# Performance work log

Hardware: AMD Instinct MI355X
Metric: run time of the kernel (lower is better)

## Reference

```python
import jax, jax.numpy as jnp
import numpy as np

L, N, HID, HEADS, BLK = 4096, 2, 1024, 16, 64
RAND_NUM = 2


def setup_inputs() -> dict:
    key = jax.random.key(0)
    ks = jax.random.split(key, 11)
    s = 0.02
    nb = L // BLK
    return {
        "query": jax.random.normal(ks[0], (L, N, HID), jnp.float32),
        "q_proj": jax.random.normal(ks[1], (HID, HID), jnp.float32) * s,
        "q_bias": jax.random.normal(ks[2], (HID,), jnp.float32) * s,
        "k_proj": jax.random.normal(ks[3], (HID, HID), jnp.float32) * s,
        "k_bias": jax.random.normal(ks[4], (HID,), jnp.float32) * s,
        "v_proj": jax.random.normal(ks[5], (HID, HID), jnp.float32) * s,
        "v_bias": jax.random.normal(ks[6], (HID,), jnp.float32) * s,
        "out_proj": jax.random.normal(ks[7], (HID, HID), jnp.float32) * s,
        "out_bias": jax.random.normal(ks[8], (HID,), jnp.float32) * s,
        "rand_indices": jax.random.randint(ks[9], (nb - 2, RAND_NUM), 2, nb, jnp.int64 if jax.config.jax_enable_x64 else jnp.int32),
        "h": HEADS,
        "block_size": BLK,
    }


def reference(query, q_proj, q_bias, k_proj, k_bias, v_proj, v_bias,
              out_proj, out_bias, rand_indices, h, block_size):
    Lq, Nb, hidden = query.shape
    dh = hidden // h
    b = block_size
    nb = Lq // b
    Z = Nb * h  # batch*heads leading dim
    scale = dh ** -0.5

    lin = lambda x, w, bi: x @ w.T + bi
    # [L, N, hidden] -> [N*h, L, dh]
    q = lin(query, q_proj, q_bias).reshape(Lq, Z, dh).transpose(1, 0, 2) * scale
    k = lin(query, k_proj, k_bias).reshape(Lq, Z, dh).transpose(1, 0, 2)
    v = lin(query, v_proj, v_bias).reshape(Lq, Z, dh).transpose(1, 0, 2)

    qb = q.reshape(Z, nb, b, dh)
    kb = k.reshape(Z, nb, b, dh)
    vb = v.reshape(Z, nb, b, dh)

    # ---- global blocks: first 2 blocks of queries attend to everything;
    #      all middle queries attend to first 2 key blocks ----
    head = jnp.einsum('zqd,zkd->zqk', q[:, :2 * b], k)          # [Z, 2b, L]
    col = jnp.einsum('zqd,zkd->zqk', q[:, 2 * b:], k[:, :2 * b])  # [Z, L-2b, 2b]

    # ---- sliding window (3 neighboring blocks), bottom row zero-padded ----
    skeys = jnp.concatenate([kb[:, 1:-2], kb[:, 2:-1], kb[:, 3:]], axis=2)  # [Z, nb-3, 3b, dh]
    sbot_k = jnp.concatenate([jnp.zeros_like(kb[:, -1:]), kb[:, -2:-1], kb[:, -1:]], axis=2)
    skeys = jnp.concatenate([skeys, sbot_k], axis=1)            # [Z, nb-2, 3b, dh]
    sqk = jnp.einsum('znqd,znkd->znqk', qb[:, 2:], skeys)
    sqk = sqk.reshape(Z, (nb - 2) * b, 3 * b)

    # ---- random blocks (rand_num per query block) ----
    gk = kb[:, rand_indices].reshape(Z, nb - 2, RAND_NUM * b, dh)
    rqk = jnp.einsum('znqd,znkd->znqk', qb[:, 2:], gk)
    rqk = rqk.reshape(Z, (nb - 2) * b, RAND_NUM * b)

    middle = jnp.concatenate([col, sqk, rqk], axis=-1)          # [Z, L-2b, 7b]

    head_attn = jax.nn.softmax(head, axis=-1)
    mid_attn = jax.nn.softmax(middle, axis=-1)

    # ---- attn @ v ----
    head_out = jnp.einsum('zqk,zkd->zqd', head_attn, v)          # [Z, 2b, dh]
    mid_out = jnp.einsum('zqk,zkd->zqd', mid_attn[:, :, :2 * b], v[:, :2 * b])

    svals = jnp.concatenate([vb[:, 1:-2], vb[:, 2:-1], vb[:, 3:]], axis=2)
    sbot_v = jnp.concatenate([vb[:, -2:-1], vb[:, -1:], jnp.zeros_like(vb[:, -1:])], axis=2)
    svals = jnp.concatenate([svals, sbot_v], axis=1)             # [Z, nb-2, 3b, dh]
    ms = mid_attn[:, :, 2 * b:5 * b].reshape(Z, nb - 2, b, 3 * b)
    mid_out = mid_out + jnp.einsum('znqk,znkd->znqd', ms, svals).reshape(Z, (nb - 2) * b, dh)

    gv = vb[:, rand_indices].reshape(Z, nb - 2, RAND_NUM * b, dh)
    mr = mid_attn[:, :, 5 * b:].reshape(Z, nb - 2, b, RAND_NUM * b)
    mid_out = mid_out + jnp.einsum('znqk,znkd->znqd', mr, gv).reshape(Z, (nb - 2) * b, dh)

    out = jnp.concatenate([head_out, mid_out], axis=1)           # [Z, L, dh]
    out = out.transpose(1, 0, 2).reshape(Lq, Nb, hidden)
    return lin(out, out_proj, out_bias)
```

## Files before the change

kernel.cpp:

```cpp
#include <hip/hip_runtime.h>
#include <stdint.h>

#define L_SEQ 4096
#define NBATCH 2
#define HID 1024
#define HEADS 16
#define DH 64
#define Z_DIM 32
#define NBLK 64
#define NROWS 8192
#define NSPLIT 8

typedef float f32x4 __attribute__((ext_vector_type(4)));
typedef short short8 __attribute__((ext_vector_type(8)));

typedef const uint32_t __attribute__((address_space(1))) *gas_ptr;
typedef uint32_t __attribute__((address_space(3))) *las_ptr;

__device__ __forceinline__ ushort f2bf(float f) {
  uint32_t u = __float_as_uint(f);
  uint32_t r = (u + 0x7FFFu + ((u >> 16) & 1u)) >> 16;
  return (ushort)r;
}

__device__ __forceinline__ void gload_lds16(const void* g, void* l) {
  __builtin_amdgcn_global_load_lds((gas_ptr)g, (las_ptr)l, 16, 0, 0);
}

__global__ __launch_bounds__(256)
void cvt_multi(const float* __restrict__ s0, ushort* __restrict__ d0,
               const float* __restrict__ s1, ushort* __restrict__ d1,
               const float* __restrict__ s2, ushort* __restrict__ d2,
               const float* __restrict__ s3, ushort* __restrict__ d3,
               const float* __restrict__ s4, ushort* __restrict__ d4) {
  const int i = blockIdx.x * blockDim.x + threadIdx.x;
  const int NQ = NROWS * HID / 4;
  const float4* src; ushort4* dst; int off;
  if (i < NQ) {
    src = (const float4*)s0; dst = (ushort4*)d0; off = i;
  } else {
    const int j = i - NQ;
    const int r = j >> 18;
    off = j & ((1 << 18) - 1);
    src = (const float4*)(r == 0 ? s1 : r == 1 ? s2 : r == 2 ? s3 : s4);
    dst = (ushort4*)(r == 0 ? d1 : r == 1 ? d2 : r == 2 ? d3 : d4);
  }
  float4 v = src[off];
  ushort4 o;
  o.x = f2bf(v.x); o.y = f2bf(v.y); o.z = f2bf(v.z); o.w = f2bf(v.w);
  dst[off] = o;
}

template <int FINAL>
__global__ __launch_bounds__(256)
void gemm_bt(const ushort* __restrict__ X,
             const ushort* __restrict__ W0, const ushort* __restrict__ W1,
             const ushort* __restrict__ W2,
             const float* __restrict__ b0, const float* __restrict__ b1,
             const float* __restrict__ b2,
             ushort* __restrict__ Qo, ushort* __restrict__ Ko,
             ushort* __restrict__ Vo, float* __restrict__ Fo) {
  const int tid = threadIdx.x;
  const int w = tid >> 6, l = tid & 63;
  const int lr = l & 15, lg = l >> 4;
  const int wr = w >> 1, wc = w & 1;

  const int total = FINAL ? 512 : 1536;
  const int per = total >> 3;
  const int f0 = blockIdx.x;
  const int nf = (f0 & 7) * per + (f0 >> 3);
  const int bx = nf & 7;
  const int by = (nf >> 3) & 63;
  const int zid = FINAL ? 0 : (nf >> 9);
  const int mbase = by * 128;
  const int nbase = bx * 128;

  const ushort* W = FINAL ? W0 : (zid == 0 ? W0 : (zid == 1 ? W1 : W2));
  const float*  B = FINAL ? b0 : (zid == 0 ? b0 : (zid == 1 ? b1 : b2));

  __shared__ ushort lds[2][8192];

  const int kch = (lg ^ ((lr >> 1) & 3)) << 3;

  f32x4 acc[4][4];
#pragma unroll
  for (int m = 0; m < 4; ++m)
#pragma unroll
    for (int n = 0; n < 4; ++n) acc[m][n] = (f32x4){0.f, 0.f, 0.f, 0.f};

  auto stage = [&](int k0, int buf) {
#pragma unroll
    for (int s = 0; s < 2; ++s) {
      const int chunk = s * 256 + tid;
      const int row = chunk >> 2, cc = chunk & 3;
      const int scc = cc ^ ((row >> 1) & 3);
      gload_lds16(X + (size_t)(mbase + row) * HID + k0 + scc * 8,
                  &lds[buf][(s * 256 + (tid & ~63)) * 8]);
      gload_lds16(W + (size_t)(nbase + row) * HID + k0 + scc * 8,
                  &lds[buf][4096 + (s * 256 + (tid & ~63)) * 8]);
    }
  };

  auto compute_tile = [&](const ushort* lA, const ushort* lB) {
    short8 af[4], bfr[4];
#pragma unroll
    for (int m = 0; m < 4; ++m)
      af[m] = *(const short8*)&lA[(wr * 64 + m * 16 + lr) * 32 + kch];
#pragma unroll
    for (int n = 0; n < 4; ++n)
      bfr[n] = *(const short8*)&lB[(wc * 64 + n * 16 + lr) * 32 + kch];
#pragma unroll
    for (int m = 0; m < 4; ++m)
#pragma unroll
      for (int n = 0; n < 4; ++n)
        acc[m][n] = __builtin_amdgcn_mfma_f32_16x16x32_bf16(af[m], bfr[n], acc[m][n], 0, 0, 0);
  };

  stage(0, 0);
  stage(32, 1);
  for (int t = 0; t < 32; ++t) {
    if (t < 30) { asm volatile("s_waitcnt vmcnt(4)" ::: "memory"); }
    else        { asm volatile("s_waitcnt vmcnt(0)" ::: "memory"); }
    __builtin_amdgcn_s_barrier();
    __builtin_amdgcn_sched_barrier(0);
    compute_tile(&lds[t & 1][0], &lds[t & 1][4096]);
    __builtin_amdgcn_sched_barrier(0);
    asm volatile("s_waitcnt lgkmcnt(0)" ::: "memory");
    __builtin_amdgcn_s_barrier();
    if (t < 30) stage((t + 2) * 32, t & 1);
  }

  if (FINAL) {
#pragma unroll
    for (int n = 0; n < 4; ++n) {
      const int col = nbase + wc * 64 + n * 16 + lr;
      const float bias = B[col];
#pragma unroll
      for (int m = 0; m < 4; ++m)
#pragma unroll
        for (int r = 0; r < 4; ++r) {
          const int row = mbase + wr * 64 + m * 16 + 4 * lg + r;
          Fo[(size_t)row * HID + col] = acc[m][n][r] + bias;
        }
    }
    return;
  }

  float biasn[4];
#pragma unroll
  for (int n = 0; n < 4; ++n) biasn[n] = B[nbase + wc * 64 + n * 16 + lr];
  ushort* st = &lds[0][0];

  if (zid == 2) {
#pragma unroll
    for (int nb2 = 0; nb2 < 2; ++nb2) {
#pragma unroll
      for (int ch = 0; ch < 2; ++ch) {
        __syncthreads();
        if (wc == ch) {
#pragma unroll
          for (int m = 0; m < 4; ++m)
#pragma unroll
            for (int n = 0; n < 4; ++n)
#pragma unroll
              for (int rr = 0; rr < 2; ++rr) {
                const int r = nb2 + 2 * rr;
                st[(n * 16 + lr) * 72 + wr * 32 + m * 8 + 2 * lg + rr] =
                    f2bf(acc[m][n][r] + biasn[n]);
              }
        }
        __syncthreads();
        const int zz = nb2 * HEADS + (nbase >> 6) + ch;
#pragma unroll
        for (int it = 0; it < 2; ++it) {
          const int c = it * 256 + tid;
          const int colI = c >> 3, ls0 = (c & 7) * 8;
          const short8 v = *(const short8*)&st[colI * 72 + ls0];
          *(short8*)&Vo[((size_t)zz * DH + colI) * L_SEQ + (mbase >> 1) + ls0] = v;
        }
      }
    }
  } else {
    ushort* Out = (zid == 0) ? Qo : Ko;
    const float sc = (zid == 0) ? 0.125f : 1.f;
#pragma unroll
    for (int nbp = 0; nbp < 2; ++nbp) {
#pragma unroll
      for (int hh = 0; hh < 2; ++hh) {
        __syncthreads();
        if (wc == hh) {
#pragma unroll
          for (int m = 0; m < 4; ++m)
#pragma unroll
            for (int n = 0; n < 4; ++n)
#pragma unroll
              for (int rr = 0; rr < 2; ++rr) {
                const int r = nbp + 2 * rr;
                st[(wr * 32 + m * 8 + 2 * lg + rr) * 72 + n * 16 + lr] =
                    f2bf((acc[m][n][r] + biasn[n]) * sc);
              }
        }
        __syncthreads();
        const int zz = nbp * HEADS + (nbase >> 6) + hh;
#pragma unroll
        for (int it = 0; it < 2; ++it) {
          const int c = it * 256 + tid;
          const int lr2 = c >> 3, cc8 = c & 7;
          const short8 v = *(const short8*)&st[lr2 * 72 + cc8 * 8];
          *(short8*)&Out[((size_t)zz * L_SEQ + (mbase >> 1) + lr2) * DH + cc8 * 8] = v;
        }
      }
    }
  }
}

__global__ __launch_bounds__(256)
void attn_sparse(const ushort* __restrict__ Q, const ushort* __restrict__ K,
                 const ushort* __restrict__ Vt, const int* __restrict__ rnd,
                 ushort* __restrict__ O,
                 float* __restrict__ Pp, float* __restrict__ Mp,
                 float* __restrict__ Lp) {
  const int bid = blockIdx.x;
  int z, qb, split = 0;
  bool head;
  if (bid < Z_DIM * 62) {
    z = bid / 62; qb = bid % 62 + 2; head = false;
  } else {
    const int t = bid - Z_DIM * 62;
    z = t >> 4; qb = (t >> 3) & 1; split = t & 7; head = true;
  }
  const int tid = threadIdx.x;
  const int w = tid >> 6, l = tid & 63;
  const int lr = l & 15, lg = l >> 4;

  __shared__ ushort Kl[64 * 64];
  __shared__ ushort Vl[64 * 64];
  __shared__ ushort Pl[4][16 * 64];

  const ushort* Qbase = Q + ((size_t)z * L_SEQ + qb * 64 + w * 16) * DH;
  const short8 aq0 = *(const short8*)(Qbase + lr * DH + lg * 8);
  const short8 aq1 = *(const short8*)(Qbase + lr * DH + 32 + lg * 8);

  float m[4], lsum[4];
  f32x4 accO[4];
#pragma unroll
  for (int r = 0; r < 4; ++r) { m[r] = -1e30f; lsum[r] = 0.f; }
#pragma unroll
  for (int t = 0; t < 4; ++t) accO[t] = (f32x4){0.f, 0.f, 0.f, 0.f};

  const int nslot = head ? 8 : 7;
  int sk[3] = {0, 0, 0}, sv[3] = {0, 0, 0}, rk0 = 0, rk1 = 0;
  if (!head) {
    const int i = qb - 2;
    rk0 = rnd[2 * i]; rk1 = rnd[2 * i + 1];
    if (qb < NBLK - 1) {
      sk[0] = qb - 1; sk[1] = qb; sk[2] = qb + 1;
      sv[0] = qb - 1; sv[1] = qb; sv[2] = qb + 1;
    } else {
      sk[0] = -1; sk[1] = NBLK - 2; sk[2] = NBLK - 1;
      sv[0] = NBLK - 2; sv[1] = NBLK - 1; sv[2] = -1;
    }
  }

  for (int slot = 0; slot < nslot; ++slot) {
    int ki, vi;
    if (head) { ki = split * 8 + slot; vi = ki; }
    else if (slot < 2) { ki = slot; vi = slot; }
    else if (slot < 5) { ki = sk[slot - 2]; vi = sv[slot - 2]; }
    else { ki = (slot == 5) ? rk0 : rk1; vi = ki; }

    if (slot) __syncthreads();
#pragma unroll
    for (int s = 0; s < 2; ++s) {
      const int chunk = s * 256 + tid;
      const int row = chunk >> 3, cc = chunk & 7;
      const int scc = cc ^ (row & 7);
      if (ki >= 0)
        gload_lds16(K + ((size_t)z * L_SEQ + ki * 64 + row) * DH + scc * 8,
                    &Kl[(s * 256 + (tid & ~63)) * 8]);
      if (vi >= 0)
        gload_lds16(Vt + ((size_t)z * DH + row) * L_SEQ + vi * 64 + scc * 8,
                    &Vl[(s * 256 + (tid & ~63)) * 8]);
    }
    __syncthreads();

    f32x4 sc[4];
    if (ki >= 0) {
#pragma unroll
      for (int t = 0; t < 4; ++t) {
        const int r = t * 16 + lr;
        const short8 b0 = *(const short8*)&Kl[r * 64 + ((lg ^ (r & 7)) << 3)];
        const short8 b1 = *(const short8*)&Kl[r * 64 + (((4 + lg) ^ (r & 7)) << 3)];
        f32x4 zz = (f32x4){0.f, 0.f, 0.f, 0.f};
        sc[t] = __builtin_amdgcn_mfma_f32_16x16x32_bf16(aq0, b0, zz, 0, 0, 0);
        sc[t] = __builtin_amdgcn_mfma_f32_16x16x32_bf16(aq1, b1, sc[t], 0, 0, 0);
      }
    } else {
#pragma unroll
      for (int t = 0; t < 4; ++t) sc[t] = (f32x4){0.f, 0.f, 0.f, 0.f};
    }

#pragma unroll
    for (int r = 0; r < 4; ++r) {
      float sm = fmaxf(fmaxf(sc[0][r], sc[1][r]), fmaxf(sc[2][r], sc[3][r]));
      sm = fmaxf(sm, __shfl_xor(sm, 1));
      sm = fmaxf(sm, __shfl_xor(sm, 2));
      sm = fmaxf(sm, __shfl_xor(sm, 4));
      sm = fmaxf(sm, __shfl_xor(sm, 8));
      const float mn = fmaxf(m[r], sm);
      const float scale = __expf(m[r] - mn);
      m[r] = mn;
      lsum[r] *= scale;
#pragma unroll
      for (int t = 0; t < 4; ++t) accO[t][r] *= scale;
      float psum = 0.f;
#pragma unroll
      for (int t = 0; t < 4; ++t) {
        const float p = __expf(sc[t][r] - mn);
        sc[t][r] = p;
        psum += p;
      }
      lsum[r] += psum;
    }

    if (vi >= 0) {
      ushort* P = &Pl[w][0];
#pragma unroll
      for (int t = 0; t < 4; ++t) {
#pragma unroll
        for (int r = 0; r < 4; ++r) {
          const int prow = 4 * lg + r, pcol = lr + 16 * t;
          P[prow * 64 + (((pcol >> 3) ^ (prow & 7)) << 3) + (pcol & 7)] = f2bf(sc[t][r]);
        }
      }
      const short8 ap0 = *(const short8*)&P[lr * 64 + ((lg ^ (lr & 7)) << 3)];
      const short8 ap1 = *(const short8*)&P[lr * 64 + (((4 + lg) ^ (lr & 7)) << 3)];
#pragma unroll
      for (int t = 0; t < 4; ++t) {
        const int r = t * 16 + lr;
        const short8 bv0 = *(const short8*)&Vl[r * 64 + ((lg ^ (r & 7)) << 3)];
        const short8 bv1 = *(const short8*)&Vl[r * 64 + (((4 + lg) ^ (r & 7)) << 3)];
        accO[t] = __builtin_amdgcn_mfma_f32_16x16x32_bf16(ap0, bv0, accO[t], 0, 0, 0);
        accO[t] = __builtin_amdgcn_mfma_f32_16x16x32_bf16(ap1, bv1, accO[t], 0, 0, 0);
      }
    }
  }

#pragma unroll
  for (int r = 0; r < 4; ++r) {
    float s = lsum[r];
    s += __shfl_xor(s, 1);
    s += __shfl_xor(s, 2);
    s += __shfl_xor(s, 4);
    s += __shfl_xor(s, 8);
    lsum[r] = s;
  }

  if (!head) {
    const int nb = z >> 4, hd = z & 15;
#pragma unroll
    for (int t = 0; t < 4; ++t) {
#pragma unroll
      for (int r = 0; r < 4; ++r) {
        const int lseq = qb * 64 + w * 16 + 4 * lg + r;
        O[((size_t)lseq * NBATCH + nb) * HID + hd * 64 + lr + 16 * t] =
            f2bf(accO[t][r] / lsum[r]);
      }
    }
  } else {
    const int hbase = (qb * Z_DIM + z) * NSPLIT + split;
#pragma unroll
    for (int t = 0; t < 4; ++t) {
#pragma unroll
      for (int r = 0; r < 4; ++r) {
        const int row = w * 16 + 4 * lg + r;
        Pp[((size_t)hbase * 64 + row) * 64 + lr + 16 * t] = accO[t][r];
      }
    }
    if (lr == 0) {
#pragma unroll
      for (int r = 0; r < 4; ++r) {
        const int row = w * 16 + 4 * lg + r;
        Mp[hbase * 64 + row] = m[r];
        Lp[hbase * 64 + row] = lsum[r];
      }
    }
  }
}

__global__ __launch_bounds__(256)
void head_reduce(const float* __restrict__ Pp, const float* __restrict__ Mp,
                 const float* __restrict__ Lp, ushort* __restrict__ O) {
  const int z = blockIdx.x >> 1, qb = blockIdx.x & 1;
  const int tid = threadIdx.x;
  const int row = tid >> 2, cg = tid & 3;
  const int base = (qb * Z_DIM + z) * NSPLIT;

  float mm[NSPLIT], wgt[NSPLIT];
  float mx = -1e30f;
#pragma unroll
  for (int s = 0; s < NSPLIT; ++s) {
    mm[s] = Mp[(base + s) * 64 + row];
    mx = fmaxf(mx, mm[s]);
  }
  float denom = 0.f;
#pragma unroll
  for (int s = 0; s < NSPLIT; ++s) {
    wgt[s] = __expf(mm[s] - mx);
    denom += Lp[(base + s) * 64 + row] * wgt[s];
  }
  const float inv = 1.f / denom;

  const int nb = z >> 4, hd = z & 15;
  const int lseq = qb * 64 + row;
#pragma unroll
  for (int c = 0; c < 16; ++c) {
    const int col = cg * 16 + c;
    float acc = 0.f;
#pragma unroll
    for (int s = 0; s < NSPLIT; ++s)
      acc += Pp[((size_t)(base + s) * 64 + row) * 64 + col] * wgt[s];
    O[((size_t)lseq * NBATCH + nb) * HID + hd * 64 + col] = f2bf(acc * inv);
  }
}

extern "C" void kernel_launch(void* const* d_in, const int* in_sizes, int n_in,
                              void* d_out, int out_size, void* d_ws, size_t ws_size,
                              hipStream_t stream) {
  (void)in_sizes; (void)n_in; (void)out_size; (void)ws_size;
  const float* query    = (const float*)d_in[0];
  const float* q_proj   = (const float*)d_in[1];
  const float* q_bias   = (const float*)d_in[2];
  const float* k_proj   = (const float*)d_in[3];
  const float* k_bias   = (const float*)d_in[4];
  const float* v_proj   = (const float*)d_in[5];
  const float* v_bias   = (const float*)d_in[6];
  const float* out_proj = (const float*)d_in[7];
  const float* out_bias = (const float*)d_in[8];
  const int*   rnd      = (const int*)d_in[9];

  ushort* Xb  = (ushort*)d_ws;
  ushort* Wq  = Xb + (size_t)NROWS * HID;
  ushort* Wk  = Wq + (size_t)HID * HID;
  ushort* Wv  = Wk + (size_t)HID * HID;
  ushort* Wo  = Wv + (size_t)HID * HID;
  ushort* Qb  = Wo + (size_t)HID * HID;
  ushort* Kb  = Qb + (size_t)Z_DIM * L_SEQ * DH;
  ushort* Vtb = Kb + (size_t)Z_DIM * L_SEQ * DH;
  float*  Pp  = (float*)(Vtb + (size_t)Z_DIM * DH * L_SEQ);
  float*  Mp  = Pp + (size_t)2 * Z_DIM * NSPLIT * 64 * 64;
  float*  Lp  = Mp + (size_t)2 * Z_DIM * NSPLIT * 64;
  ushort* Ob  = Xb;
  float*  Fo  = (float*)d_out;

  cvt_multi<<<(NROWS * HID / 4 + 4 * HID * HID / 4) / 256, 256, 0, stream>>>(
      query, Xb, q_proj, Wq, k_proj, Wk, v_proj, Wv, out_proj, Wo);

  gemm_bt<0><<<1536, 256, 0, stream>>>(
      Xb, Wq, Wk, Wv, q_bias, k_bias, v_bias, Qb, Kb, Vtb, nullptr);

  attn_sparse<<<Z_DIM * 62 + 2 * Z_DIM * NSPLIT, 256, 0, stream>>>(
      Qb, Kb, Vtb, rnd, Ob, Pp, Mp, Lp);

  head_reduce<<<2 * Z_DIM, 256, 0, stream>>>(Pp, Mp, Lp, Ob);

  gemm_bt<1><<<512, 256, 0, stream>>>(
      Ob, Wo, nullptr, nullptr, out_bias, nullptr, nullptr,
      nullptr, nullptr, nullptr, Fo);
}
```

Before: 172.4 us.

## Double-buffer K/V LDS tiles in sparse attention with prefetch two slots ahead

Splits the K and V shared-memory tiles into two buffers and issues direct-to-LDS loads for the next two slots ahead, using explicit vmcnt waits and raw barriers. Global loads can then overlap the QK and PV MFMA work instead of stalling at a sync on every slot. It also raises wave priority around the MFMA sections. Invalid block indices (-1) are clamped to block 0, so extra loads are issued and later ignored. The change doubles K/V LDS use and relies on hand-counted vmcnt values being correct.

```diff
diff --git a/kernel.cpp b/kernel.cpp
--- a/kernel.cpp
+++ b/kernel.cpp
@@ -233,8 +233,8 @@
   const int w = tid >> 6, l = tid & 63;
   const int lr = l & 15, lg = l >> 4;
 
-  __shared__ ushort Kl[64 * 64];
-  __shared__ ushort Vl[64 * 64];
+  __shared__ ushort Kl[2][64 * 64];
+  __shared__ ushort Vl[2][64 * 64];
   __shared__ ushort Pl[4][16 * 64];
 
   const ushort* Qbase = Q + ((size_t)z * L_SEQ + qb * 64 + w * 16) * DH;
@@ -262,39 +262,53 @@
     }
   }
 
-  for (int slot = 0; slot < nslot; ++slot) {
-    int ki, vi;
+  auto slot_kv = [&](int slot, int& ki, int& vi) {
     if (head) { ki = split * 8 + slot; vi = ki; }
     else if (slot < 2) { ki = slot; vi = slot; }
     else if (slot < 5) { ki = sk[slot - 2]; vi = sv[slot - 2]; }
     else { ki = (slot == 5) ? rk0 : rk1; vi = ki; }
-
-    if (slot) __syncthreads();
+  };
+
+  auto stage = [&](int slot, int buf) {
+    int ki, vi; slot_kv(slot, ki, vi);
+    const int kiL = ki < 0 ? 0 : ki;
+    const int viL = vi < 0 ? 0 : vi;
 #pragma unroll
     for (int s = 0; s < 2; ++s) {
       const int chunk = s * 256 + tid;
       const int row = chunk >> 3, cc = chunk & 7;
       const int scc = cc ^ (row & 7);
-      if (ki >= 0)
-        gload_lds16(K + ((size_t)z * L_SEQ + ki * 64 + row) * DH + scc * 8,
-                    &Kl[(s * 256 + (tid & ~63)) * 8]);
-      if (vi >= 0)
-        gload_lds16(Vt + ((size_t)z * DH + row) * L_SEQ + vi * 64 + scc * 8,
-                    &Vl[(s * 256 + (tid & ~63)) * 8]);
-    }
-    __syncthreads();
+      gload_lds16(K + ((size_t)z * L_SEQ + kiL * 64 + row) * DH + scc * 8,
+                  &Kl[buf][(s * 256 + (tid & ~63)) * 8]);
+      gload_lds16(Vt + ((size_t)z * DH + row) * L_SEQ + viL * 64 + scc * 8,
+                  &Vl[buf][(s * 256 + (tid & ~63)) * 8]);
+    }
+  };
+
+  stage(0, 0);
+  stage(1, 1);
+
+  for (int slot = 0; slot < nslot; ++slot) {
+    int ki, vi; slot_kv(slot, ki, vi);
+    const int buf = slot & 1;
+    if (slot < nslot - 1) { asm volatile("s_waitcnt vmcnt(4)" ::: "memory"); }
+    else                  { asm volatile("s_waitcnt vmcnt(0)" ::: "memory"); }
+    __builtin_amdgcn_s_barrier();
+    __builtin_amdgcn_sched_barrier(0);
 
     f32x4 sc[4];
     if (ki >= 0) {
+      __builtin_amdgcn_s_setprio(1);
 #pragma unroll
       for (int t = 0; t < 4; ++t) {
         const int r = t * 16 + lr;
-        const short8 b0 = *(const short8*)&Kl[r * 64 + ((lg ^ (r & 7)) << 3)];
-        const short8 b1 = *(const short8*)&Kl[r * 64 + (((4 + lg) ^ (r & 7)) << 3)];
+        const short8 b0 = *(const short8*)&Kl[buf][r * 64 + ((lg ^ (r & 7)) << 3)];
+        const short8 b1 = *(const short8*)&Kl[buf][r * 64 + (((4 + lg) ^ (r & 7)) << 3)];
         f32x4 zz = (f32x4){0.f, 0.f, 0.f, 0.f};
         sc[t] = __builtin_amdgcn_mfma_f32_16x16x32_bf16(aq0, b0, zz, 0, 0, 0);
         sc[t] = __builtin_amdgcn_mfma_f32_16x16x32_bf16(aq1, b1, sc[t], 0, 0, 0);
       }
+      __builtin_amdgcn_s_setprio(0);
     } else {
 #pragma unroll
       for (int t = 0; t < 4; ++t) sc[t] = (f32x4){0.f, 0.f, 0.f, 0.f};
@@ -335,15 +349,22 @@
       }
       const short8 ap0 = *(const short8*)&P[lr * 64 + ((lg ^ (lr & 7)) << 3)];
       const short8 ap1 = *(const short8*)&P[lr * 64 + (((4 + lg) ^ (lr & 7)) << 3)];
+      __builtin_amdgcn_s_setprio(1);
 #pragma unroll
       for (int t = 0; t < 4; ++t) {
         const int r = t * 16 + lr;
-        const short8 bv0 = *(const short8*)&Vl[r * 64 + ((lg ^ (r & 7)) << 3)];
-        const short8 bv1 = *(const short8*)&Vl[r * 64 + (((4 + lg) ^ (r & 7)) << 3)];
+        const short8 bv0 = *(const short8*)&Vl[buf][r * 64 + ((lg ^ (r & 7)) << 3)];
+        const short8 bv1 = *(const short8*)&Vl[buf][r * 64 + (((4 + lg) ^ (r & 7)) << 3)];
         accO[t] = __builtin_amdgcn_mfma_f32_16x16x32_bf16(ap0, bv0, accO[t], 0, 0, 0);
         accO[t] = __builtin_amdgcn_mfma_f32_16x16x32_bf16(ap1, bv1, accO[t], 0, 0, 0);
       }
-    }
+      __builtin_amdgcn_s_setprio(0);
+    }
+
+    __builtin_amdgcn_sched_barrier(0);
+    asm volatile("s_waitcnt lgkmcnt(0)" ::: "memory");
+    __builtin_amdgcn_s_barrier();
+    if (slot + 2 < nslot) stage(slot + 2, buf);
   }
 
 #pragma unroll
```

New measurement: 180.7 us. +4.8%, slower.

## Compute transposed scores in registers and drop LDS staging in sparse attention

Applied to the files above, without the earlier changes.

The sparse attention kernel now computes S^T = K·Q^T, so each lane owns one query row. Softmax max and sum then need only two cross-lane shuffles, and each lane keeps a scalar m/lsum. K and V tiles are loaded straight from global memory into registers, which removes the LDS staging and the per-slot __syncthreads. P is repacked for the PV MFMA with packed bf16 converts and lane shuffles instead of a round trip through shared memory, and the output and partial stores become vectorized. In exchange, each wave loads K/V on its own with no sharing across the 4 waves, which adds global/L2 traffic, and the loads are no longer overlapped.

```diff
diff --git a/kernel.cpp b/kernel.cpp
--- a/kernel.cpp
+++ b/kernel.cpp
@@ -21,6 +21,12 @@
   uint32_t u = __float_as_uint(f);
   uint32_t r = (u + 0x7FFFu + ((u >> 16) & 1u)) >> 16;
   return (ushort)r;
+}
+
+__device__ __forceinline__ uint32_t cvtpk(float a, float b) {
+  uint32_t r;
+  asm("v_cvt_pk_bf16_f32 %0, %1, %2" : "=v"(r) : "v"(a), "v"(b));
+  return r;
 }
 
 __device__ __forceinline__ void gload_lds16(const void* g, void* l) {
@@ -233,20 +239,14 @@
   const int w = tid >> 6, l = tid & 63;
   const int lr = l & 15, lg = l >> 4;
 
-  __shared__ ushort Kl[64 * 64];
-  __shared__ ushort Vl[64 * 64];
-  __shared__ ushort Pl[4][16 * 64];
-
-  const ushort* Qbase = Q + ((size_t)z * L_SEQ + qb * 64 + w * 16) * DH;
-  const short8 aq0 = *(const short8*)(Qbase + lr * DH + lg * 8);
-  const short8 aq1 = *(const short8*)(Qbase + lr * DH + 32 + lg * 8);
-
-  float m[4], lsum[4];
+  const ushort* Qrow = Q + ((size_t)z * L_SEQ + qb * 64 + w * 16 + lr) * DH;
+  const short8 bq0 = *(const short8*)(Qrow + lg * 8);
+  const short8 bq1 = *(const short8*)(Qrow + 32 + lg * 8);
+
+  float m = -1e30f, lsum = 0.f;
   f32x4 accO[4];
 #pragma unroll
-  for (int r = 0; r < 4; ++r) { m[r] = -1e30f; lsum[r] = 0.f; }
-#pragma unroll
-  for (int t = 0; t < 4; ++t) accO[t] = (f32x4){0.f, 0.f, 0.f, 0.f};
+  for (int td = 0; td < 4; ++td) accO[td] = (f32x4){0.f, 0.f, 0.f, 0.f};
 
   const int nslot = head ? 8 : 7;
   int sk[3] = {0, 0, 0}, sv[3] = {0, 0, 0}, rk0 = 0, rk1 = 0;
@@ -262,6 +262,10 @@
     }
   }
 
+  const int srcA = lr + 16 * (2 * (lg & 1));
+  const int srcB = srcA + 16;
+  const bool hiTile = ((lg >> 1) & 1) != 0;
+
   for (int slot = 0; slot < nslot; ++slot) {
     int ki, vi;
     if (head) { ki = split * 8 + slot; vi = ki; }
@@ -269,121 +273,114 @@
     else if (slot < 5) { ki = sk[slot - 2]; vi = sv[slot - 2]; }
     else { ki = (slot == 5) ? rk0 : rk1; vi = ki; }
 
-    if (slot) __syncthreads();
-#pragma unroll
-    for (int s = 0; s < 2; ++s) {
-      const int chunk = s * 256 + tid;
-      const int row = chunk >> 3, cc = chunk & 7;
-      const int scc = cc ^ (row & 7);
-      if (ki >= 0)
-        gload_lds16(K + ((size_t)z * L_SEQ + ki * 64 + row) * DH + scc * 8,
-                    &Kl[(s * 256 + (tid & ~63)) * 8]);
-      if (vi >= 0)
-        gload_lds16(Vt + ((size_t)z * DH + row) * L_SEQ + vi * 64 + scc * 8,
-                    &Vl[(s * 256 + (tid & ~63)) * 8]);
-    }
-    __syncthreads();
-
     f32x4 sc[4];
     if (ki >= 0) {
+      const ushort* Kbase = K + ((size_t)z * L_SEQ + ki * 64) * DH;
+      short8 aK[4][2];
 #pragma unroll
       for (int t = 0; t < 4; ++t) {
-        const int r = t * 16 + lr;
-        const short8 b0 = *(const short8*)&Kl[r * 64 + ((lg ^ (r & 7)) << 3)];
-        const short8 b1 = *(const short8*)&Kl[r * 64 + (((4 + lg) ^ (r & 7)) << 3)];
+        aK[t][0] = *(const short8*)(Kbase + (t * 16 + lr) * DH + lg * 8);
+        aK[t][1] = *(const short8*)(Kbase + (t * 16 + lr) * DH + 32 + lg * 8);
+      }
+#pragma unroll
+      for (int t = 0; t < 4; ++t) {
         f32x4 zz = (f32x4){0.f, 0.f, 0.f, 0.f};
-        sc[t] = __builtin_amdgcn_mfma_f32_16x16x32_bf16(aq0, b0, zz, 0, 0, 0);
-        sc[t] = __builtin_amdgcn_mfma_f32_16x16x32_bf16(aq1, b1, sc[t], 0, 0, 0);
+        sc[t] = __builtin_amdgcn_mfma_f32_16x16x32_bf16(aK[t][0], bq0, zz, 0, 0, 0);
+        sc[t] = __builtin_amdgcn_mfma_f32_16x16x32_bf16(aK[t][1], bq1, sc[t], 0, 0, 0);
       }
     } else {
 #pragma unroll
       for (int t = 0; t < 4; ++t) sc[t] = (f32x4){0.f, 0.f, 0.f, 0.f};
     }
 
-#pragma unroll
-    for (int r = 0; r < 4; ++r) {
-      float sm = fmaxf(fmaxf(sc[0][r], sc[1][r]), fmaxf(sc[2][r], sc[3][r]));
-      sm = fmaxf(sm, __shfl_xor(sm, 1));
-      sm = fmaxf(sm, __shfl_xor(sm, 2));
-      sm = fmaxf(sm, __shfl_xor(sm, 4));
-      sm = fmaxf(sm, __shfl_xor(sm, 8));
-      const float mn = fmaxf(m[r], sm);
-      const float scale = __expf(m[r] - mn);
-      m[r] = mn;
-      lsum[r] *= scale;
-#pragma unroll
-      for (int t = 0; t < 4; ++t) accO[t][r] *= scale;
-      float psum = 0.f;
-#pragma unroll
-      for (int t = 0; t < 4; ++t) {
+    short8 av[4][2];
+    if (vi >= 0) {
+      const ushort* Vbase = Vt + (size_t)z * DH * L_SEQ + vi * 64;
+#pragma unroll
+      for (int td = 0; td < 4; ++td) {
+        av[td][0] = *(const short8*)(Vbase + (size_t)(td * 16 + lr) * L_SEQ + lg * 8);
+        av[td][1] = *(const short8*)(Vbase + (size_t)(td * 16 + lr) * L_SEQ + 32 + lg * 8);
+      }
+    }
+
+    float sm = sc[0][0];
+#pragma unroll
+    for (int t = 0; t < 4; ++t)
+#pragma unroll
+      for (int r = 0; r < 4; ++r) sm = fmaxf(sm, sc[t][r]);
+    sm = fmaxf(sm, __shfl_xor(sm, 16));
+    sm = fmaxf(sm, __shfl_xor(sm, 32));
+    const float mn = fmaxf(m, sm);
+    const float scale = __expf(m - mn);
+    m = mn;
+    lsum *= scale;
+#pragma unroll
+    for (int td = 0; td < 4; ++td)
+#pragma unroll
+      for (int r = 0; r < 4; ++r) accO[td][r] *= scale;
+    float psum = 0.f;
+#pragma unroll
+    for (int t = 0; t < 4; ++t)
+#pragma unroll
+      for (int r = 0; r < 4; ++r) {
         const float p = __expf(sc[t][r] - mn);
         sc[t][r] = p;
         psum += p;
       }
-      lsum[r] += psum;
-    }
+    psum += __shfl_xor(psum, 16);
+    psum += __shfl_xor(psum, 32);
+    lsum += psum;
 
     if (vi >= 0) {
-      ushort* P = &Pl[w][0];
+      uint32_t pk[4][2];
 #pragma unroll
       for (int t = 0; t < 4; ++t) {
-#pragma unroll
-        for (int r = 0; r < 4; ++r) {
-          const int prow = 4 * lg + r, pcol = lr + 16 * t;
-          P[prow * 64 + (((pcol >> 3) ^ (prow & 7)) << 3) + (pcol & 7)] = f2bf(sc[t][r]);
-        }
-      }
-      const short8 ap0 = *(const short8*)&P[lr * 64 + ((lg ^ (lr & 7)) << 3)];
-      const short8 ap1 = *(const short8*)&P[lr * 64 + (((4 + lg) ^ (lr & 7)) << 3)];
-#pragma unroll
-      for (int t = 0; t < 4; ++t) {
-        const int r = t * 16 + lr;
-        const short8 bv0 = *(const short8*)&Vl[r * 64 + ((lg ^ (r & 7)) << 3)];
-        const short8 bv1 = *(const short8*)&Vl[r * 64 + (((4 + lg) ^ (r & 7)) << 3)];
-        accO[t] = __builtin_amdgcn_mfma_f32_16x16x32_bf16(ap0, bv0, accO[t], 0, 0, 0);
-        accO[t] = __builtin_amdgcn_mfma_f32_16x16x32_bf16(ap1, bv1, accO[t], 0, 0, 0);
-      }
-    }
-  }
-
-#pragma unroll
-  for (int r = 0; r < 4; ++r) {
-    float s = lsum[r];
-    s += __shfl_xor(s, 1);
-    s += __shfl_xor(s, 2);
-    s += __shfl_xor(s, 4);
-    s += __shfl_xor(s, 8);
-    lsum[r] = s;
+        pk[t][0] = cvtpk(sc[t][0], sc[t][1]);
+        pk[t][1] = cvtpk(sc[t][2], sc[t][3]);
+      }
+#pragma unroll
+      for (int f = 0; f < 2; ++f) {
+        uint32_t u[4];
+        const int tl = 2 * f, th = 2 * f + 1;
+        const uint32_t a0 = __shfl((int)pk[tl][0], srcA), b0 = __shfl((int)pk[th][0], srcA);
+        const uint32_t a1 = __shfl((int)pk[tl][1], srcA), b1 = __shfl((int)pk[th][1], srcA);
+        const uint32_t a2 = __shfl((int)pk[tl][0], srcB), b2 = __shfl((int)pk[th][0], srcB);
+        const uint32_t a3 = __shfl((int)pk[tl][1], srcB), b3 = __shfl((int)pk[th][1], srcB);
+        u[0] = hiTile ? b0 : a0;
+        u[1] = hiTile ? b1 : a1;
+        u[2] = hiTile ? b2 : a2;
+        u[3] = hiTile ? b3 : a3;
+        union { uint32_t u4[4]; short8 s8; } cv;
+        cv.u4[0] = u[0]; cv.u4[1] = u[1]; cv.u4[2] = u[2]; cv.u4[3] = u[3];
+        const short8 pb = cv.s8;
+#pragma unroll
+        for (int td = 0; td < 4; ++td)
+          accO[td] = __builtin_amdgcn_mfma_f32_16x16x32_bf16(av[td][f], pb, accO[td], 0, 0, 0);
+      }
+    }
   }
 
   if (!head) {
+    const float inv = 1.f / lsum;
     const int nb = z >> 4, hd = z & 15;
-#pragma unroll
-    for (int t = 0; t < 4; ++t) {
-#pragma unroll
-      for (int r = 0; r < 4; ++r) {
-        const int lseq = qb * 64 + w * 16 + 4 * lg + r;
-        O[((size_t)lseq * NBATCH + nb) * HID + hd * 64 + lr + 16 * t] =
-            f2bf(accO[t][r] / lsum[r]);
-      }
+    const size_t rowbase =
+        ((size_t)(qb * 64 + w * 16 + lr) * NBATCH + nb) * HID + hd * 64;
+#pragma unroll
+    for (int td = 0; td < 4; ++td) {
+      uint2 o;
+      o.x = cvtpk(accO[td][0] * inv, accO[td][1] * inv);
+      o.y = cvtpk(accO[td][2] * inv, accO[td][3] * inv);
+      *(uint2*)&O[rowbase + td * 16 + 4 * lg] = o;
     }
   } else {
     const int hbase = (qb * Z_DIM + z) * NSPLIT + split;
-#pragma unroll
-    for (int t = 0; t < 4; ++t) {
-#pragma unroll
-      for (int r = 0; r < 4; ++r) {
-        const int row = w * 16 + 4 * lg + r;
-        Pp[((size_t)hbase * 64 + row) * 64 + lr + 16 * t] = accO[t][r];
-      }
-    }
-    if (lr == 0) {
-#pragma unroll
-      for (int r = 0; r < 4; ++r) {
-        const int row = w * 16 + 4 * lg + r;
-        Mp[hbase * 64 + row] = m[r];
-        Lp[hbase * 64 + row] = lsum[r];
-      }
+    const size_t prow = (size_t)hbase * 64 + w * 16 + lr;
+#pragma unroll
+    for (int td = 0; td < 4; ++td)
+      *(f32x4*)&Pp[prow * 64 + td * 16 + 4 * lg] = accO[td];
+    if (l < 16) {
+      Mp[hbase * 64 + w * 16 + lr] = m;
+      Lp[hbase * 64 + w * 16 + lr] = lsum;
     }
   }
 }
```

After: 252.7 us. 1.47x slower.
